# Kernel tuning notes

Measured on AMD Instinct MI355X. Metric: run time of the kernel, lower is better.

Reference implementation:

```python
import jax, jax.numpy as jnp
import numpy as np

N = 100000
E = 1600000
IN_C, HID_C, OUT_C = 128, 64, 40


def setup_inputs() -> dict:
    key = jax.random.key(0)
    ks = jax.random.split(key, 9)
    x = jax.random.normal(ks[0], (N, IN_C), dtype=jnp.float32)
    src = jax.random.randint(ks[1], (E,), 0, N, dtype=jnp.int64)
    dst = jax.random.randint(ks[2], (E,), 0, N, dtype=jnp.int64)
    edge_index = jnp.stack([src, dst], axis=0)
    def glorot(k, fan_in, fan_out):
        s = jnp.sqrt(6.0 / (fan_in + fan_out)).astype(jnp.float32)
        return jax.random.uniform(k, (fan_in, fan_out), jnp.float32, -s, s)
    return {
        "x": x,
        "edge_index": edge_index,
        "W1": glorot(ks[3], IN_C, HID_C), "b1": jnp.zeros((HID_C,), jnp.float32),
        "W2": glorot(ks[4], HID_C, HID_C), "b2": jnp.zeros((HID_C,), jnp.float32),
        "W3": glorot(ks[5], HID_C, OUT_C), "b3": jnp.zeros((OUT_C,), jnp.float32),
    }


def _gcn_norm(edge_index, n_nodes):
    # add self-loops, then symmetric normalization D^-1/2 (A+I) D^-1/2
    loops = jnp.arange(n_nodes, dtype=edge_index.dtype)
    src = jnp.concatenate([edge_index[0], loops])
    dst = jnp.concatenate([edge_index[1], loops])
    deg = jax.ops.segment_sum(jnp.ones_like(dst, dtype=jnp.float32), dst,
                              num_segments=n_nodes)
    dinv = jnp.where(deg > 0, jax.lax.rsqrt(deg), 0.0)
    norm = dinv[src] * dinv[dst]  # [E + N]
    return src, dst, norm


def _gcn_conv(h, W, b, src, dst, norm, n_nodes):
    h = h @ W                                   # [N, out]
    msg = norm[:, None] * h[src]                # gather + scale, [E+N, out]
    out = jax.ops.segment_sum(msg, dst, num_segments=n_nodes)  # scatter-add
    return out + b


def reference(x, edge_index, W1, b1, W2, b2, W3, b3):
    n_nodes = x.shape[0]
    src, dst, norm = _gcn_norm(edge_index, n_nodes)
    h = jax.nn.relu(_gcn_conv(x, W1, b1, src, dst, norm, n_nodes))
    # dropout(p=0.5) is identity in eval mode
    h = jax.nn.relu(_gcn_conv(h, W2, b2, src, dst, norm, n_nodes))
    out = _gcn_conv(h, W3, b3, src, dst, norm, n_nodes)
    return out
```

## Files before the change

kernel.cpp:

```cpp
#include <hip/hip_runtime.h>

#define N_NODES 100000
#define N_EDGES 1600000
#define NBUCK 196
#define BCAP 9600
#define CH 4096
#define NCHUNK ((N_EDGES + CH - 1) / CH)

typedef __attribute__((ext_vector_type(2))) _Float16 half2v;
typedef __attribute__((ext_vector_type(4))) _Float16 half4v;
typedef __attribute__((ext_vector_type(8))) _Float16 half8v;
typedef __attribute__((ext_vector_type(4))) float f32x4;

__device__ __forceinline__ float4 loadX4(const float* X, size_t idx) {
    return *(const float4*)(X + idx);
}
__device__ __forceinline__ float4 loadX4(const _Float16* X, size_t idx) {
    half4v h = *(const half4v*)(X + idx);
    return make_float4((float)h.x, (float)h.y, (float)h.z, (float)h.w);
}


__global__ __launch_bounds__(256) void zero_small(int* p, int n) {
    int i = blockIdx.x * blockDim.x + threadIdx.x;
    if (i < n) p[i] = 0;
}

__global__ __launch_bounds__(256) void multisplit(const int* __restrict__ src,
                                                  const int* __restrict__ dst,
                                                  int* cursor,
                                                  int* __restrict__ bucketed, int e) {
    __shared__ int cnt[NBUCK];
    __shared__ int basel[NBUCK];
    const int t = threadIdx.x;
    const int base_e = blockIdx.x * CH;

    int myS[16], myD[16];
    for (int i = t; i < NBUCK; i += 256) cnt[i] = 0;
    __syncthreads();

#pragma unroll
    for (int k = 0; k < 16; ++k) {
        int i = base_e + k * 256 + t;
        if (i < e) {
            myS[k] = src[i];
            myD[k] = dst[i];
            atomicAdd(&cnt[myD[k] >> 9], 1);
        } else {
            myD[k] = -1;
        }
    }
    __syncthreads();
    for (int i = t; i < NBUCK; i += 256) basel[i] = atomicAdd(&cursor[i], cnt[i]);
    __syncthreads();
    for (int i = t; i < NBUCK; i += 256) cnt[i] = 0;
    __syncthreads();

#pragma unroll
    for (int k = 0; k < 16; ++k) {
        if (myD[k] >= 0) {
            int b = myD[k] >> 9;
            int pos = basel[b] + atomicAdd(&cnt[b], 1);
            if (pos < BCAP)
                bucketed[(size_t)b * BCAP + pos] = ((myD[k] & 511) << 17) | myS[k];
        }
    }
}

__global__ __launch_bounds__(256) void bucket_scan(const int* __restrict__ cursor,
                                                   int* __restrict__ gbase) {
    __shared__ int sm[256];
    const int t = threadIdx.x;
    int v = (t < NBUCK) ? cursor[t] : 0;
    sm[t] = v;
    __syncthreads();
    for (int off = 1; off < 256; off <<= 1) {
        int u = (t >= off) ? sm[t - off] : 0;
        __syncthreads();
        sm[t] += u;
        __syncthreads();
    }
    if (t < NBUCK) gbase[t] = sm[t] - v;
    if (t == NBUCK - 1) gbase[NBUCK] = sm[t];
}

__global__ __launch_bounds__(512) void build_csr(const int* __restrict__ bucketed,
                                                 const int* __restrict__ gbase,
                                                 int* __restrict__ row_ptr,
                                                 float* __restrict__ dinv,
                                                 int* __restrict__ csr_src, int n) {
    __shared__ int vals[BCAP];
    __shared__ int cnt[512];
    __shared__ int lcur[512];
    const int b = blockIdx.x;
    const int t = threadIdx.x;
    const int nb0 = b * 512;
    const int nn = min(512, n - nb0);
    const int gb = gbase[b];
    const int m = gbase[b + 1] - gb;

    cnt[t] = 0;
    __syncthreads();
    for (int i = t; i < m; i += 512) {
        int v = bucketed[(size_t)b * BCAP + i];
        vals[i] = v;
        atomicAdd(&cnt[v >> 17], 1);
    }
    __syncthreads();

    int deg = cnt[t];
    for (int off = 1; off < 512; off <<= 1) {
        int u = (t >= off) ? cnt[t - off] : 0;
        __syncthreads();
        cnt[t] += u;
        __syncthreads();
    }
    int offv = cnt[t] - deg;
    __syncthreads();
    cnt[t] = offv;
    lcur[t] = 0;
    if (t < nn) {
        row_ptr[nb0 + t] = gb + offv;
        dinv[nb0 + t] = rsqrtf((float)(deg + 1));
    }
    if (b == NBUCK - 1 && t == 0) row_ptr[n] = gb + m;
    __syncthreads();

    for (int i = t; i < m; i += 512) {
        int v = vals[i];
        int node = v >> 17;
        int pos = atomicAdd(&lcur[node], 1);
        csr_src[gb + cnt[node] + pos] = v & 0x1FFFF;
    }
}


template <int K>
__global__ __launch_bounds__(256) void transpose_w(const float* __restrict__ W,
                                                   _Float16* __restrict__ Wt) {
    int i = blockIdx.x * 256 + threadIdx.x;
    if (i < K * 64) {
        int k = i >> 6, nn = i & 63;
        Wt[(size_t)nn * K + k] = (_Float16)W[i];
    }
}


__device__ __forceinline__ void stageX_rows(const float* X, _Float16* Xl, int t,
                                            int row0, int n, int K, int SP) {
    for (int i = t; i < 64 * K / 4; i += 256) {
        int r = i / (K / 4), c = (i % (K / 4)) * 4;
        int grow = min(row0 + r, n - 1);
        float4 v = *(const float4*)(X + (size_t)grow * K + c);
        half4v h = {(_Float16)v.x, (_Float16)v.y, (_Float16)v.z, (_Float16)v.w};
        *(half4v*)(Xl + r * SP + c) = h;
    }
}
__device__ __forceinline__ void stageX_rows(const _Float16* X, _Float16* Xl, int t,
                                            int row0, int n, int K, int SP) {
    for (int i = t; i < 64 * K / 8; i += 256) {
        int r = i / (K / 8), c = (i % (K / 8)) * 8;
        int grow = min(row0 + r, n - 1);
        *(half8v*)(Xl + r * SP + c) = *(const half8v*)(X + (size_t)grow * K + c);
    }
}

template <int K, typename XT>
__global__ __launch_bounds__(256) void gemm_mfma64(const XT* __restrict__ X,
                                                   const _Float16* __restrict__ Wt,
                                                   const float* __restrict__ dinv,
                                                   _Float16* __restrict__ Y, int n) {
    constexpr int SP = K + 8;
    __shared__ _Float16 Xl[64 * SP];
    __shared__ _Float16 Wl[64 * SP];
    const int t = threadIdx.x;
    const int wave = t >> 6, lane = t & 63;
    const int row0 = blockIdx.x * 64;
    const int m = lane & 15, quad = lane >> 4;

    for (int i = t; i < 64 * K / 8; i += 256) {
        int r = i / (K / 8), c = (i % (K / 8)) * 8;
        *(half8v*)(Wl + r * SP + c) = *(const half8v*)(Wt + (size_t)r * K + c);
    }
    stageX_rows(X, Xl, t, row0, n, K, SP);
    __syncthreads();

    f32x4 acc[4] = {{0,0,0,0},{0,0,0,0},{0,0,0,0},{0,0,0,0}};
#pragma unroll
    for (int k0 = 0; k0 < K; k0 += 32) {
        half8v a = *(const half8v*)(Xl + (wave * 16 + m) * SP + k0 + quad * 8);
#pragma unroll
        for (int ct = 0; ct < 4; ++ct) {
            half8v b = *(const half8v*)(Wl + (ct * 16 + m) * SP + k0 + quad * 8);
            acc[ct] = __builtin_amdgcn_mfma_f32_16x16x32_f16(a, b, acc[ct], 0, 0, 0);
        }
    }

    float dv[4];
#pragma unroll
    for (int r = 0; r < 4; ++r) {
        int row = row0 + wave * 16 + quad * 4 + r;
        dv[r] = dinv[min(row, n - 1)];
    }
#pragma unroll
    for (int ct = 0; ct < 4; ++ct) {
#pragma unroll
        for (int r = 0; r < 4; ++r) {
            int row = row0 + wave * 16 + quad * 4 + r;
            if (row < n)
                Y[(size_t)row * 64 + ct * 16 + m] = (_Float16)(dv[r] * acc[ct][r]);
        }
    }
}


template <int K, int COUT, typename XT>
__global__ __launch_bounds__(256) void gemm_rt(const XT* __restrict__ X,
                                               const float* __restrict__ W,
                                               const float* __restrict__ dinv,
                                               _Float16* __restrict__ Y, int n) {
    constexpr int KC = 64;
    constexpr int S = KC + 4;
    constexpr int NCH = K / KC;
    __shared__ float Xl[64 * S];
    __shared__ float Wl[KC * COUT];

    const int t = threadIdx.x;
    const int row0 = blockIdx.x * 64;
    const int cg = (t & 15) * 4;
    const int rg = (t >> 4) * 4;

    float acc[4][4] = {};

#pragma unroll
    for (int ch = 0; ch < NCH; ++ch) {
        const int k0 = ch * KC;
        for (int i = t; i < 64 * KC / 4; i += 256) {
            int r = i >> 4;
            int k = (i & 15) * 4;
            int grow = min(row0 + r, n - 1);
            *(float4*)(Xl + r * S + k) = loadX4(X, (size_t)grow * K + k0 + k);
        }
        for (int i = t; i < KC * COUT / 4; i += 256) {
            *(float4*)(Wl + i * 4) = *(const float4*)(W + (size_t)k0 * COUT + (size_t)i * 4);
        }
        __syncthreads();

        if (cg < COUT) {
#pragma unroll 4
            for (int k = 0; k < KC; ++k) {
                float4 w = *(const float4*)(Wl + k * COUT + cg);
                float x0 = Xl[(rg + 0) * S + k];
                float x1 = Xl[(rg + 1) * S + k];
                float x2 = Xl[(rg + 2) * S + k];
                float x3 = Xl[(rg + 3) * S + k];
                acc[0][0] += x0 * w.x; acc[0][1] += x0 * w.y; acc[0][2] += x0 * w.z; acc[0][3] += x0 * w.w;
                acc[1][0] += x1 * w.x; acc[1][1] += x1 * w.y; acc[1][2] += x1 * w.z; acc[1][3] += x1 * w.w;
                acc[2][0] += x2 * w.x; acc[2][1] += x2 * w.y; acc[2][2] += x2 * w.z; acc[2][3] += x2 * w.w;
                acc[3][0] += x3 * w.x; acc[3][1] += x3 * w.y; acc[3][2] += x3 * w.z; acc[3][3] += x3 * w.w;
            }
        }
        __syncthreads();
    }

    if (cg < COUT) {
#pragma unroll
        for (int r = 0; r < 4; ++r) {
            int row = row0 + rg + r;
            if (row < n) {
                float d = dinv[row];
                half4v o = { (_Float16)(d * acc[r][0]), (_Float16)(d * acc[r][1]),
                             (_Float16)(d * acc[r][2]), (_Float16)(d * acc[r][3]) };
                *(half4v*)(Y + (size_t)row * COUT + cg) = o;
            }
        }
    }
}


template <bool RELU>
__global__ __launch_bounds__(256) void aggregate64b(const _Float16* __restrict__ tS,
                                                    const int* __restrict__ row_ptr,
                                                    const int* __restrict__ csr_src,
                                                    const float* __restrict__ dinv,
                                                    const float* __restrict__ bias,
                                                    _Float16* __restrict__ out, int n) {
    const int lane = threadIdx.x & 63;
    const int node = blockIdx.x * 4 + (threadIdx.x >> 6);
    if (node >= n) return;
    const int g = lane >> 3;
    const int c8 = lane & 7;
    const half8v* tS8 = (const half8v*)tS;

    const int beg = row_ptr[node];
    const int cnt = row_ptr[node + 1] - beg;

    half8v accA, accB;
#pragma unroll
    for (int i = 0; i < 8; ++i) { accA[i] = (_Float16)0; accB[i] = (_Float16)0; }

    for (int j0 = 0; j0 < cnt; j0 += 64) {
        const int m = min(64, cnt - j0);
        int sj = csr_src[beg + j0 + min(lane, m - 1)];

        int j = 0;
        for (; j + 16 <= m; j += 16) {
            int e0 = __shfl(sj, j + g);
            int e1 = __shfl(sj, j + 8 + g);
            half8v v0 = tS8[(size_t)e0 * 8 + c8];
            half8v v1 = tS8[(size_t)e1 * 8 + c8];
            accA += v0;
            accB += v1;
        }
        for (; j + 8 <= m; j += 8) {
            int e0 = __shfl(sj, j + g);
            accA += tS8[(size_t)e0 * 8 + c8];
        }
        if (j < m) {
            int idx = j + g;
            int e0 = __shfl(sj, min(idx, m - 1));
            half8v v = tS8[(size_t)e0 * 8 + c8];
            if (idx < m) accB += v;
        }
    }

    float acc[8];
#pragma unroll
    for (int i = 0; i < 8; ++i) acc[i] = (float)accA[i] + (float)accB[i];
#pragma unroll
    for (int off = 8; off < 64; off <<= 1) {
#pragma unroll
        for (int i = 0; i < 8; ++i) acc[i] += __shfl_xor(acc[i], off);
    }

    if (lane < 8) {
        half8v selfh = tS8[(size_t)node * 8 + c8];
        float4 b0 = *(const float4*)(bias + c8 * 8);
        float4 b1 = *(const float4*)(bias + c8 * 8 + 4);
        const float bb[8] = {b0.x, b0.y, b0.z, b0.w, b1.x, b1.y, b1.z, b1.w};
        float d = dinv[node];
        half8v o;
#pragma unroll
        for (int i = 0; i < 8; ++i) {
            float v = bb[i] + d * (acc[i] + (float)selfh[i]);
            if (RELU) v = fmaxf(v, 0.0f);
            o[i] = (_Float16)v;
        }
        ((half8v*)out)[(size_t)node * 8 + c8] = o;
    }
}


__global__ __launch_bounds__(256) void aggregate40v(const _Float16* __restrict__ tS,
                                                    const int* __restrict__ row_ptr,
                                                    const int* __restrict__ csr_src,
                                                    const float* __restrict__ dinv,
                                                    const float* __restrict__ bias,
                                                    float* __restrict__ out, int n) {
    const int lane = threadIdx.x & 63;
    const int node = blockIdx.x * 4 + (threadIdx.x >> 6);
    if (node >= n) return;
    const int g = lane / 20;
    const int c2 = lane - 20 * g;
    const bool act = (g < 3);
    const half2v* tS2 = (const half2v*)tS;

    const int beg = row_ptr[node];
    const int cnt = row_ptr[node + 1] - beg;

    half2v a0 = {(_Float16)0, (_Float16)0}, a1 = a0, a2 = a0, a3 = a0;

    for (int j0 = 0; j0 < cnt; j0 += 64) {
        const int m = min(64, cnt - j0);
        int sj = (lane < m) ? csr_src[beg + j0 + lane] : 0;

        int j = 0;
        for (; j + 12 <= m; j += 12) {
            int i0 = j + g, i1 = j + 3 + g, i2 = j + 6 + g, i3 = j + 9 + g;
            int e0 = __shfl(sj, i0 < m ? i0 : 0);
            int e1 = __shfl(sj, i1 < m ? i1 : 0);
            int e2 = __shfl(sj, i2 < m ? i2 : 0);
            int e3 = __shfl(sj, i3 < m ? i3 : 0);
            half2v v0 = tS2[(size_t)e0 * 20 + c2];
            half2v v1 = tS2[(size_t)e1 * 20 + c2];
            half2v v2 = tS2[(size_t)e2 * 20 + c2];
            half2v v3 = tS2[(size_t)e3 * 20 + c2];
            if (act) { a0 += v0; a1 += v1; a2 += v2; a3 += v3; }
        }
        for (; j + 3 <= m; j += 3) {
            int i0 = j + g;
            int e0 = __shfl(sj, i0 < m ? i0 : 0);
            half2v v0 = tS2[(size_t)e0 * 20 + c2];
            if (act) a0 += v0;
        }
        if (j < m) {
            int idx = j + g;
            int e0 = __shfl(sj, idx < m ? idx : m - 1);
            half2v v = tS2[(size_t)e0 * 20 + c2];
            if (act && idx < m) a1 += v;
        }
    }

    float2 s;
    s.x = ((float)a0.x + (float)a1.x) + ((float)a2.x + (float)a3.x);
    s.y = ((float)a0.y + (float)a1.y) + ((float)a2.y + (float)a3.y);
    float sx1 = __shfl(s.x, lane + 20), sy1 = __shfl(s.y, lane + 20);
    float sx2 = __shfl(s.x, lane + 40), sy2 = __shfl(s.y, lane + 40);
    if (lane < 20) {
        s.x += sx1 + sx2;
        s.y += sy1 + sy2;
        half2v selfh = tS2[(size_t)node * 20 + c2];
        float2 b = ((const float2*)bias)[c2];
        float d = dinv[node];
        float2 o;
        o.x = b.x + d * (s.x + (float)selfh.x);
        o.y = b.y + d * (s.y + (float)selfh.y);
        ((float2*)out)[(size_t)node * 20 + c2] = o;
    }
}


extern "C" void kernel_launch(void* const* d_in, const int* in_sizes, int n_in,
                              void* d_out, int out_size, void* d_ws, size_t ws_size,
                              hipStream_t stream) {
    const float* x  = (const float*)d_in[0];
    const int*   ei = (const int*)d_in[1];
    const int*   src = ei;
    const int*   dst = ei + N_EDGES;
    const float* W1 = (const float*)d_in[2];
    const float* b1 = (const float*)d_in[3];
    const float* W2 = (const float*)d_in[4];
    const float* b2 = (const float*)d_in[5];
    const float* W3 = (const float*)d_in[6];
    const float* b3 = (const float*)d_in[7];
    float* out = (float*)d_out;

    const int N = N_NODES, E = N_EDGES;

    char* p = (char*)d_ws;
    int*   cursor   = (int*)p;              p += 256 * 4;
    int*   gbase    = (int*)p;              p += 256 * 4;
    float* dinv     = (float*)p;            p += (size_t)N * 4;
    int*   row_ptr  = (int*)p;              p += (size_t)(N + 4) * 4;
    int*   bucketed = (int*)p;              p += (size_t)NBUCK * BCAP * 4;
    int*   csr_src  = (int*)p;              p += (size_t)E * 4;
    p = (char*)(((size_t)p + 15) & ~(size_t)15);
    _Float16* Wt1   = (_Float16*)p;         p += (size_t)64 * 128 * 2;
    _Float16* Wt2   = (_Float16*)p;         p += (size_t)64 * 64 * 2;
    _Float16* bufA  = (_Float16*)p;         p += (size_t)N * 64 * 2;
    p = (char*)(((size_t)p + 15) & ~(size_t)15);
    _Float16* bufB  = (_Float16*)p;         p += (size_t)N * 64 * 2;

    zero_small<<<1, 256, 0, stream>>>(cursor, NBUCK);
    transpose_w<128><<<32, 256, 0, stream>>>(W1, Wt1);
    transpose_w<64><<<16, 256, 0, stream>>>(W2, Wt2);
    multisplit<<<NCHUNK, 256, 0, stream>>>(src, dst, cursor, bucketed, E);
    bucket_scan<<<1, 256, 0, stream>>>(cursor, gbase);
    build_csr<<<NBUCK, 512, 0, stream>>>(bucketed, gbase, row_ptr, dinv, csr_src, N);

    const int aggGrid = (N + 3) / 4;
    const int gemmGrid = (N + 63) / 64;

    gemm_mfma64<128, float><<<gemmGrid, 256, 0, stream>>>(x, Wt1, dinv, bufA, N);
    aggregate64b<true><<<aggGrid, 256, 0, stream>>>(bufA, row_ptr, csr_src, dinv, b1, bufB, N);

    gemm_mfma64<64, _Float16><<<gemmGrid, 256, 0, stream>>>(bufB, Wt2, dinv, bufA, N);
    aggregate64b<true><<<aggGrid, 256, 0, stream>>>(bufA, row_ptr, csr_src, dinv, b2, bufB, N);

    gemm_rt<64, 40, _Float16><<<gemmGrid, 256, 0, stream>>>(bufB, W3, dinv, bufA, N);
    aggregate40v<<<aggGrid, 256, 0, stream>>>(bufA, row_ptr, csr_src, dinv, b3, out, N);
}
```

Baseline: 329.1 us.

## Use 16-byte gathers in final aggregation and halve CSR build bucket size

The last-layer aggregation now has each lane load 8 fp16 channels (half8v), so one wave covers 12 neighbors per step instead of 3, with 2 accumulators and a shuffle-tree reduction. Each gathered row now takes 5 wide loads instead of 20 narrow ones. The CSR build uses 391 buckets of 256 nodes with 256-thread blocks instead of 196 buckets of 512, which gives more blocks and less shared memory per block. It also adds an unguarded csr_src load clamped to m-1, and the smaller bucket capacity lowers the overflow headroom per bucket.

```diff
diff --git a/kernel.cpp b/kernel.cpp
--- a/kernel.cpp
+++ b/kernel.cpp
@@ -2,8 +2,8 @@
 
 #define N_NODES 100000
 #define N_EDGES 1600000
-#define NBUCK 196
-#define BCAP 9600
+#define NBUCK 391
+#define BCAP 4800
 #define CH 4096
 #define NCHUNK ((N_EDGES + CH - 1) / CH)
 
@@ -45,7 +45,7 @@
         if (i < e) {
             myS[k] = src[i];
             myD[k] = dst[i];
-            atomicAdd(&cnt[myD[k] >> 9], 1);
+            atomicAdd(&cnt[myD[k] >> 8], 1);
         } else {
             myD[k] = -1;
         }
@@ -59,22 +59,22 @@
 #pragma unroll
     for (int k = 0; k < 16; ++k) {
         if (myD[k] >= 0) {
-            int b = myD[k] >> 9;
+            int b = myD[k] >> 8;
             int pos = basel[b] + atomicAdd(&cnt[b], 1);
             if (pos < BCAP)
-                bucketed[(size_t)b * BCAP + pos] = ((myD[k] & 511) << 17) | myS[k];
-        }
-    }
-}
-
-__global__ __launch_bounds__(256) void bucket_scan(const int* __restrict__ cursor,
+                bucketed[(size_t)b * BCAP + pos] = ((myD[k] & 255) << 17) | myS[k];
+        }
+    }
+}
+
+__global__ __launch_bounds__(512) void bucket_scan(const int* __restrict__ cursor,
                                                    int* __restrict__ gbase) {
-    __shared__ int sm[256];
+    __shared__ int sm[512];
     const int t = threadIdx.x;
     int v = (t < NBUCK) ? cursor[t] : 0;
     sm[t] = v;
     __syncthreads();
-    for (int off = 1; off < 256; off <<= 1) {
+    for (int off = 1; off < 512; off <<= 1) {
         int u = (t >= off) ? sm[t - off] : 0;
         __syncthreads();
         sm[t] += u;
@@ -84,24 +84,24 @@
     if (t == NBUCK - 1) gbase[NBUCK] = sm[t];
 }
 
-__global__ __launch_bounds__(512) void build_csr(const int* __restrict__ bucketed,
+__global__ __launch_bounds__(256) void build_csr(const int* __restrict__ bucketed,
                                                  const int* __restrict__ gbase,
                                                  int* __restrict__ row_ptr,
                                                  float* __restrict__ dinv,
                                                  int* __restrict__ csr_src, int n) {
     __shared__ int vals[BCAP];
-    __shared__ int cnt[512];
-    __shared__ int lcur[512];
+    __shared__ int cnt[256];
+    __shared__ int lcur[256];
     const int b = blockIdx.x;
     const int t = threadIdx.x;
-    const int nb0 = b * 512;
-    const int nn = min(512, n - nb0);
+    const int nb0 = b * 256;
+    const int nn = min(256, n - nb0);
     const int gb = gbase[b];
     const int m = gbase[b + 1] - gb;
 
     cnt[t] = 0;
     __syncthreads();
-    for (int i = t; i < m; i += 512) {
+    for (int i = t; i < m; i += 256) {
         int v = bucketed[(size_t)b * BCAP + i];
         vals[i] = v;
         atomicAdd(&cnt[v >> 17], 1);
@@ -109,7 +109,7 @@
     __syncthreads();
 
     int deg = cnt[t];
-    for (int off = 1; off < 512; off <<= 1) {
+    for (int off = 1; off < 256; off <<= 1) {
         int u = (t >= off) ? cnt[t - off] : 0;
         __syncthreads();
         cnt[t] += u;
@@ -126,7 +126,7 @@
     if (b == NBUCK - 1 && t == 0) row_ptr[n] = gb + m;
     __syncthreads();
 
-    for (int i = t; i < m; i += 512) {
+    for (int i = t; i < m; i += 256) {
         int v = vals[i];
         int node = v >> 17;
         int pos = atomicAdd(&lcur[node], 1);
@@ -351,7 +351,7 @@
 }
 
 
-__global__ __launch_bounds__(256) void aggregate40v(const _Float16* __restrict__ tS,
+__global__ __launch_bounds__(256) void aggregate40b(const _Float16* __restrict__ tS,
                                                     const int* __restrict__ row_ptr,
                                                     const int* __restrict__ csr_src,
                                                     const float* __restrict__ dinv,
@@ -360,62 +360,68 @@
     const int lane = threadIdx.x & 63;
     const int node = blockIdx.x * 4 + (threadIdx.x >> 6);
     if (node >= n) return;
-    const int g = lane / 20;
-    const int c2 = lane - 20 * g;
-    const bool act = (g < 3);
-    const half2v* tS2 = (const half2v*)tS;
+    const int g = lane / 5;
+    const int c5 = lane - 5 * g;
+    const bool act = (g < 12);
+    const half8v* tS8 = (const half8v*)tS;
 
     const int beg = row_ptr[node];
     const int cnt = row_ptr[node + 1] - beg;
 
-    half2v a0 = {(_Float16)0, (_Float16)0}, a1 = a0, a2 = a0, a3 = a0;
+    half8v accA, accB;
+#pragma unroll
+    for (int i = 0; i < 8; ++i) { accA[i] = (_Float16)0; accB[i] = (_Float16)0; }
 
     for (int j0 = 0; j0 < cnt; j0 += 64) {
         const int m = min(64, cnt - j0);
-        int sj = (lane < m) ? csr_src[beg + j0 + lane] : 0;
+        int sj = csr_src[beg + j0 + min(lane, m - 1)];
 
         int j = 0;
+        for (; j + 24 <= m; j += 24) {
+            int e0 = __shfl(sj, j + g);
+            int e1 = __shfl(sj, j + 12 + g);
+            half8v v0 = tS8[(size_t)e0 * 5 + c5];
+            half8v v1 = tS8[(size_t)e1 * 5 + c5];
+            if (act) { accA += v0; accB += v1; }
+        }
         for (; j + 12 <= m; j += 12) {
-            int i0 = j + g, i1 = j + 3 + g, i2 = j + 6 + g, i3 = j + 9 + g;
-            int e0 = __shfl(sj, i0 < m ? i0 : 0);
-            int e1 = __shfl(sj, i1 < m ? i1 : 0);
-            int e2 = __shfl(sj, i2 < m ? i2 : 0);
-            int e3 = __shfl(sj, i3 < m ? i3 : 0);
-            half2v v0 = tS2[(size_t)e0 * 20 + c2];
-            half2v v1 = tS2[(size_t)e1 * 20 + c2];
-            half2v v2 = tS2[(size_t)e2 * 20 + c2];
-            half2v v3 = tS2[(size_t)e3 * 20 + c2];
-            if (act) { a0 += v0; a1 += v1; a2 += v2; a3 += v3; }
-        }
-        for (; j + 3 <= m; j += 3) {
-            int i0 = j + g;
-            int e0 = __shfl(sj, i0 < m ? i0 : 0);
-            half2v v0 = tS2[(size_t)e0 * 20 + c2];
-            if (act) a0 += v0;
+            int e0 = __shfl(sj, j + g);
+            half8v v0 = tS8[(size_t)e0 * 5 + c5];
+            if (act) accA += v0;
         }
         if (j < m) {
             int idx = j + g;
-            int e0 = __shfl(sj, idx < m ? idx : m - 1);
-            half2v v = tS2[(size_t)e0 * 20 + c2];
-            if (act && idx < m) a1 += v;
-        }
-    }
-
-    float2 s;
-    s.x = ((float)a0.x + (float)a1.x) + ((float)a2.x + (float)a3.x);
-    s.y = ((float)a0.y + (float)a1.y) + ((float)a2.y + (float)a3.y);
-    float sx1 = __shfl(s.x, lane + 20), sy1 = __shfl(s.y, lane + 20);
-    float sx2 = __shfl(s.x, lane + 40), sy2 = __shfl(s.y, lane + 40);
-    if (lane < 20) {
-        s.x += sx1 + sx2;
-        s.y += sy1 + sy2;
-        half2v selfh = tS2[(size_t)node * 20 + c2];
-        float2 b = ((const float2*)bias)[c2];
+            int e0 = __shfl(sj, min(idx, m - 1));
+            half8v v = tS8[(size_t)e0 * 5 + c5];
+            if (act && idx < m) accB += v;
+        }
+    }
+
+    float acc[8];
+#pragma unroll
+    for (int i = 0; i < 8; ++i) acc[i] = (float)accA[i] + (float)accB[i];
+#pragma unroll
+    for (int i = 0; i < 8; ++i) {
+        acc[i] += __shfl(acc[i], lane + 30);
+        acc[i] += __shfl(acc[i], lane + 15);
+        float p1 = __shfl(acc[i], lane + 5);
+        float p2 = __shfl(acc[i], lane + 10);
+        acc[i] += p1 + p2;
+    }
+
+    if (lane < 5) {
+        half8v selfh = tS8[(size_t)node * 5 + c5];
+        float4 b0 = *(const float4*)(bias + c5 * 8);
+        float4 b1 = *(const float4*)(bias + c5 * 8 + 4);
+        const float bb[8] = {b0.x, b0.y, b0.z, b0.w, b1.x, b1.y, b1.z, b1.w};
         float d = dinv[node];
-        float2 o;
-        o.x = b.x + d * (s.x + (float)selfh.x);
-        o.y = b.y + d * (s.y + (float)selfh.y);
-        ((float2*)out)[(size_t)node * 20 + c2] = o;
+        float ov[8];
+#pragma unroll
+        for (int i = 0; i < 8; ++i)
+            ov[i] = bb[i] + d * (acc[i] + (float)selfh[i]);
+        float4* o4 = (float4*)(out + (size_t)node * 40 + c5 * 8);
+        o4[0] = make_float4(ov[0], ov[1], ov[2], ov[3]);
+        o4[1] = make_float4(ov[4], ov[5], ov[6], ov[7]);
     }
 }
 
@@ -438,8 +444,8 @@
     const int N = N_NODES, E = N_EDGES;
 
     char* p = (char*)d_ws;
-    int*   cursor   = (int*)p;              p += 256 * 4;
-    int*   gbase    = (int*)p;              p += 256 * 4;
+    int*   cursor   = (int*)p;              p += 512 * 4;
+    int*   gbase    = (int*)p;              p += 512 * 4;
     float* dinv     = (float*)p;            p += (size_t)N * 4;
     int*   row_ptr  = (int*)p;              p += (size_t)(N + 4) * 4;
     int*   bucketed = (int*)p;              p += (size_t)NBUCK * BCAP * 4;
@@ -451,12 +457,12 @@
     p = (char*)(((size_t)p + 15) & ~(size_t)15);
     _Float16* bufB  = (_Float16*)p;         p += (size_t)N * 64 * 2;
 
-    zero_small<<<1, 256, 0, stream>>>(cursor, NBUCK);
+    zero_small<<<2, 256, 0, stream>>>(cursor, NBUCK);
     transpose_w<128><<<32, 256, 0, stream>>>(W1, Wt1);
     transpose_w<64><<<16, 256, 0, stream>>>(W2, Wt2);
     multisplit<<<NCHUNK, 256, 0, stream>>>(src, dst, cursor, bucketed, E);
-    bucket_scan<<<1, 256, 0, stream>>>(cursor, gbase);
-    build_csr<<<NBUCK, 512, 0, stream>>>(bucketed, gbase, row_ptr, dinv, csr_src, N);
+    bucket_scan<<<1, 512, 0, stream>>>(cursor, gbase);
+    build_csr<<<NBUCK, 256, 0, stream>>>(bucketed, gbase, row_ptr, dinv, csr_src, N);
 
     const int aggGrid = (N + 3) / 4;
     const int gemmGrid = (N + 63) / 64;
@@ -468,5 +474,5 @@
     aggregate64b<true><<<aggGrid, 256, 0, stream>>>(bufA, row_ptr, csr_src, dinv, b2, bufB, N);
 
     gemm_rt<64, 40, _Float16><<<gemmGrid, 256, 0, stream>>>(bufB, W3, dinv, bufA, N);
-    aggregate40v<<<aggGrid, 256, 0, stream>>>(bufA, row_ptr, csr_src, dinv, b3, out, N);
-}
+    aggregate40b<<<aggGrid, 256, 0, stream>>>(bufA, row_ptr, csr_src, dinv, b3, out, N);
+}
```

Result: no change. 331.3 us (+0.6%).
